# Performance work log

Hardware: AMD Instinct MI355X
Metric: run time of the kernel (lower is better)

The kernel has to match this reference:

```python
import jax, jax.numpy as jnp
import numpy as np

N_FULL = 50000
N_POOL = 12500
E_FULL = 600000
E_POOL = 150000
D = 128


def gcn_conv(x, W, b, edge_index, n):
    """GCNConv with self-loops and symmetric normalization.
    x: [n, d_in], W: [d_in, d_out], edge_index: [2, E] (src -> dst)."""
    xw = x @ W  # [n, d_out]
    loops = jnp.arange(n, dtype=edge_index.dtype)
    src = jnp.concatenate([edge_index[0], loops])
    dst = jnp.concatenate([edge_index[1], loops])
    deg = jnp.zeros((n,), dtype=xw.dtype).at[dst].add(1.0)  # >= 1 (self loops)
    dinv = jax.lax.rsqrt(deg)
    norm = (dinv[src] * dinv[dst])[:, None]  # [E+n, 1]
    out = jax.ops.segment_sum(xw[src] * norm, dst, num_segments=n)
    return out + b


def setup_inputs() -> dict:
    key = jax.random.key(0)
    ks = jax.random.split(key, 8)
    s = 1.0 / np.sqrt(D)
    return {
        "x": jnp.zeros((N_FULL, D), jnp.float32),
        "edge_index": jax.random.randint(ks[0], (2, E_FULL), 0, N_FULL, dtype=jnp.int64)
            if jax.config.jax_enable_x64 else jax.random.randint(ks[0], (2, E_FULL), 0, N_FULL).astype(jnp.int32),
        "pooled_x": jax.random.normal(ks[1], (N_POOL, D), jnp.float32),
        "pooled_edge_index": jax.random.randint(ks[2], (2, E_POOL), 0, N_POOL).astype(jnp.int32),
        "unpool_info": jnp.arange(N_POOL, dtype=jnp.int32),  # unique TopK-kept indices
        "W0": jax.random.normal(ks[3], (D, D), jnp.float32) * s,
        "b0": jnp.zeros((D,), jnp.float32),
        "W1": jax.random.normal(ks[4], (D, D), jnp.float32) * s,
        "b1": jnp.zeros((D,), jnp.float32),
        "W2": jax.random.normal(ks[5], (D, D), jnp.float32) * s,
        "b2": jnp.zeros((D,), jnp.float32),
    }


def reference(x, edge_index, pooled_x, pooled_edge_index, unpool_info,
              W0, b0, W1, b1, W2, b2):
    n = x.shape[0]
    # conv0 on the pooled graph + activation (ELU)
    h = jax.nn.elu(gcn_conv(pooled_x, W0, b0, pooled_edge_index, pooled_x.shape[0]))
    # TopKPool unpool: zero full graph, scatter pooled features to kept indices
    xf = jnp.zeros_like(x).at[unpool_info].set(h)
    # remaining convs on the full graph (dropout=0 / eval mode -> identity)
    xf = jax.nn.elu(gcn_conv(xf, W1, b1, edge_index, n))
    xf = jax.nn.elu(gcn_conv(xf, W2, b2, edge_index, n))
    return xf
```

## Files before the change

### kernel.cpp

```cpp
#include <hip/hip_runtime.h>
#include <math.h>

#define DD 128

static inline int cdiv(long a, long b){ return (int)((a + b - 1) / b); }

typedef __attribute__((ext_vector_type(4))) float f32x4;
typedef __attribute__((ext_vector_type(8))) short bf16x8;
typedef __attribute__((ext_vector_type(4))) short sh4;

__device__ __forceinline__ unsigned short bf16_rn(float f){
  unsigned u = __float_as_uint(f);
  u += 0x7fffu + ((u >> 16) & 1u);
  return (unsigned short)(u >> 16);
}

__global__ void k_count2(const int* __restrict__ dst_f, int Ef, int* __restrict__ cnt_f,
                         int* __restrict__ rank_f,
                         const int* __restrict__ dst_p, int Ep, int* __restrict__ cnt_p,
                         int* __restrict__ rank_p,
                         int* __restrict__ invm, int nf){
  int e = blockIdx.x * blockDim.x + threadIdx.x;
  if (e < Ef){ rank_f[e] = atomicAdd(&cnt_f[dst_f[e]], 1); return; }
  e -= Ef;
  if (e < Ep){ rank_p[e] = atomicAdd(&cnt_p[dst_p[e]], 1); return; }
  e -= Ep;
  if (e < nf) invm[e] = -1;
}

__global__ __launch_bounds__(256) void k_bsum(
    const int* __restrict__ cnt_f, int nf, const int* __restrict__ cnt_p, int np,
    int* __restrict__ bsum_f, int* __restrict__ bsum_p, int nbf, int nbp,
    const int* __restrict__ unpool, int* __restrict__ inv, int npool){
  int bi = blockIdx.x;
  if (bi >= nbf + nbp){
    int i = (bi - nbf - nbp) * 256 + threadIdx.x;
    if (i < npool) inv[unpool[i]] = i;
    return;
  }
  const int* cnt; int n; int* bsum; int b;
  if (bi < nbf){ cnt = cnt_f; n = nf; bsum = bsum_f; b = bi; }
  else         { cnt = cnt_p; n = np; bsum = bsum_p; b = bi - nbf; }
  __shared__ int s[256];
  int t = threadIdx.x;
  long base = (long)b * 1024 + t * 4;
  int v = 0;
  if (base + 3 < n){ int4 q = *(const int4*)(cnt + base); v = q.x + q.y + q.z + q.w; }
  else { for (int j = 0; j < 4; j++) if (base + j < n) v += cnt[base + j]; }
  s[t] = v; __syncthreads();
  for (int off = 128; off > 0; off >>= 1){ if (t < off) s[t] += s[t + off]; __syncthreads(); }
  if (t == 0) bsum[b] = s[0];
}

__global__ __launch_bounds__(128) void k_scan_b(int* __restrict__ bsum_f, int nbf,
                                                int* __restrict__ bsum_p, int nbp){
  __shared__ int s[128];
  int t = threadIdx.x;
  int v = (t < nbf) ? bsum_f[t] : 0;
  s[t] = v; __syncthreads();
  for (int off = 1; off < 128; off <<= 1){ int u = (t >= off) ? s[t - off] : 0; __syncthreads(); s[t] += u; __syncthreads(); }
  if (t < nbf) bsum_f[t] = s[t] - v;
  __syncthreads();
  int v2 = (t < nbp) ? bsum_p[t] : 0;
  s[t] = v2; __syncthreads();
  for (int off = 1; off < 128; off <<= 1){ int u = (t >= off) ? s[t - off] : 0; __syncthreads(); s[t] += u; __syncthreads(); }
  if (t < nbp) bsum_p[t] = s[t] - v2;
}

__global__ __launch_bounds__(256) void k_scan_f(
    const int* __restrict__ cnt_f, int nf, const int* __restrict__ bsum_f,
    const int* __restrict__ cnt_p, int np, const int* __restrict__ bsum_p,
    int* __restrict__ rptr_f, float* __restrict__ dinv_f,
    int* __restrict__ rptr_p, float* __restrict__ dinv_p,
    int nbf, int Ef, int Ep){
  const int* cnt; const int* bsum; int* rptr; float* dinv; int n; int b;
  if ((int)blockIdx.x < nbf){ cnt=cnt_f; bsum=bsum_f; rptr=rptr_f; dinv=dinv_f; n=nf; b=blockIdx.x; }
  else                      { cnt=cnt_p; bsum=bsum_p; rptr=rptr_p; dinv=dinv_p; n=np; b=blockIdx.x-nbf; }
  __shared__ int s[256];
  int t = threadIdx.x;
  long base = (long)b * 1024 + t * 4;
  int c0=0,c1=0,c2=0,c3=0;
  if (base + 3 < n){ int4 q = *(const int4*)(cnt + base); c0=q.x; c1=q.y; c2=q.z; c3=q.w; }
  else {
    if (base + 0 < n) c0 = cnt[base + 0];
    if (base + 1 < n) c1 = cnt[base + 1];
    if (base + 2 < n) c2 = cnt[base + 2];
  }
  int tsum = c0 + c1 + c2 + c3;
  s[t] = tsum; __syncthreads();
  for (int off = 1; off < 256; off <<= 1){ int u = (t >= off) ? s[t - off] : 0; __syncthreads(); s[t] += u; __syncthreads(); }
  int run = bsum[b] + s[t] - tsum;
  int r0 = run, r1 = r0 + c0, r2 = r1 + c1, r3 = r2 + c2;
  if (base + 3 < n){
    *(int4*)(rptr + base) = make_int4(r0, r1, r2, r3);
    dinv[base + 0] = rsqrtf((float)(c0 + 1));
    dinv[base + 1] = rsqrtf((float)(c1 + 1));
    dinv[base + 2] = rsqrtf((float)(c2 + 1));
    dinv[base + 3] = rsqrtf((float)(c3 + 1));
  } else {
    if (base + 0 < n){ rptr[base+0]=r0; dinv[base+0]=rsqrtf((float)(c0+1)); }
    if (base + 1 < n){ rptr[base+1]=r1; dinv[base+1]=rsqrtf((float)(c1+1)); }
    if (base + 2 < n){ rptr[base+2]=r2; dinv[base+2]=rsqrtf((float)(c2+1)); }
  }
  if (blockIdx.x == 0 && t == 0){ rptr_f[nf] = Ef; rptr_p[np] = Ep; }
}

__global__ void k_fill2(const int* __restrict__ src_f, const int* __restrict__ dst_f, int Ef,
                        const int* __restrict__ rptr_f, const int* __restrict__ rank_f,
                        int2* __restrict__ ewk1_f, int2* __restrict__ ewk2_f,
                        const float* __restrict__ dinv_f, const int* __restrict__ inv,
                        const int* __restrict__ src_p, const int* __restrict__ dst_p, int Ep,
                        const int* __restrict__ rptr_p, const int* __restrict__ rank_p,
                        int2* __restrict__ ewk_p,
                        const float* __restrict__ dinv_p){
  int e = blockIdx.x * blockDim.x + threadIdx.x;
  if (e < Ef){
    int s = src_f[e];
    int p = rptr_f[dst_f[e]] + rank_f[e];
    int w = __float_as_int(dinv_f[s]);
    ewk2_f[p] = make_int2(s, w);
    ewk1_f[p] = make_int2(inv[s], w);
  } else {
    e -= Ef;
    if (e < Ep){
      int s = src_p[e];
      int p = rptr_p[dst_p[e]] + rank_p[e];
      ewk_p[p] = make_int2(s, __float_as_int(dinv_p[s]));
    }
  }
}

template <bool BF16OUT>
__global__ __launch_bounds__(256, 2) void k_gemm_mfma(const float* __restrict__ A,
                                                      const float* __restrict__ W,
                                                      void* __restrict__ Cout, int n){
  __shared__ unsigned short Wl[2][16384];
  const int t    = threadIdx.x;
  const int lane = t & 63;
  const int wv   = t >> 6;
  const int g    = lane >> 4;
  const int r    = lane & 15;

  #pragma unroll
  for (int i = 0; i < 4; i++){
    int item = t + i * 256;
    int kq = item >> 5;
    int c4 = item & 31;
    const float* Wp = W + (long)kq * 512 + c4 * 4;
    float4 ww[4];
    #pragma unroll
    for (int kk = 0; kk < 4; kk++) ww[kk] = *(const float4*)(Wp + kk * 128);
    #pragma unroll
    for (int m = 0; m < 4; m++){
      int c = c4 * 4 + m;
      int boff = c * 256 + (((kq >> 1) ^ (c & 15)) * 16) + (kq & 1) * 8;
      sh4 hq, lq;
      #pragma unroll
      for (int kk = 0; kk < 4; kk++){
        float f = ((const float*)&ww[kk])[m];
        unsigned short hh = bf16_rn(f);
        float hf = __uint_as_float((unsigned)hh << 16);
        hq[kk] = (short)hh;
        lq[kk] = (short)bf16_rn(f - hf);
      }
      *(sh4*)((char*)(&Wl[0][0]) + boff) = hq;
      *(sh4*)((char*)(&Wl[1][0]) + boff) = lq;
    }
  }
  __syncthreads();

  const int rb = blockIdx.x * 128 + wv * 32;
  const int r0 = rb + r, r1 = rb + 16 + r;
  const bool v0 = r0 < n, v1 = r1 < n;
  const float* pa0 = A + (long)r0 * DD + g * 8;
  const float* pa1 = A + (long)r1 * DD + g * 8;

  f32x4 acc[2][8];
  #pragma unroll
  for (int i = 0; i < 2; i++)
    #pragma unroll
    for (int j = 0; j < 8; j++){ f32x4 z = {0.f,0.f,0.f,0.f}; acc[i][j] = z; }

  #pragma unroll
  for (int ks = 0; ks < 4; ks++){
    const float4 z4 = make_float4(0.f,0.f,0.f,0.f);
    float4 a00 = v0 ? *(const float4*)(pa0 + ks * 32)     : z4;
    float4 a01 = v0 ? *(const float4*)(pa0 + ks * 32 + 4) : z4;
    float4 a10 = v1 ? *(const float4*)(pa1 + ks * 32)     : z4;
    float4 a11 = v1 ? *(const float4*)(pa1 + ks * 32 + 4) : z4;
    bf16x8 ah0, al0, ah1, al1;
    {
      float f[8] = {a00.x,a00.y,a00.z,a00.w,a01.x,a01.y,a01.z,a01.w};
      #pragma unroll
      for (int i = 0; i < 8; i++){
        unsigned short hh = bf16_rn(f[i]);
        ah0[i] = (short)hh;
        al0[i] = (short)bf16_rn(f[i] - __uint_as_float((unsigned)hh << 16));
      }
    }
    {
      float f[8] = {a10.x,a10.y,a10.z,a10.w,a11.x,a11.y,a11.z,a11.w};
      #pragma unroll
      for (int i = 0; i < 8; i++){
        unsigned short hh = bf16_rn(f[i]);
        ah1[i] = (short)hh;
        al1[i] = (short)bf16_rn(f[i] - __uint_as_float((unsigned)hh << 16));
      }
    }
    const int sb = ks * 4 + g;
    #pragma unroll
    for (int cf = 0; cf < 8; cf++){
      const int boff = (cf * 16 + r) * 256 + ((sb ^ r) * 16);
      bf16x8 wh = *(const bf16x8*)((const char*)(&Wl[0][0]) + boff);
      bf16x8 wl = *(const bf16x8*)((const char*)(&Wl[1][0]) + boff);
      acc[0][cf] = __builtin_amdgcn_mfma_f32_16x16x32_bf16(ah0, wh, acc[0][cf], 0, 0, 0);
      acc[1][cf] = __builtin_amdgcn_mfma_f32_16x16x32_bf16(ah1, wh, acc[1][cf], 0, 0, 0);
      acc[0][cf] = __builtin_amdgcn_mfma_f32_16x16x32_bf16(al0, wh, acc[0][cf], 0, 0, 0);
      acc[1][cf] = __builtin_amdgcn_mfma_f32_16x16x32_bf16(al1, wh, acc[1][cf], 0, 0, 0);
      acc[0][cf] = __builtin_amdgcn_mfma_f32_16x16x32_bf16(ah0, wl, acc[0][cf], 0, 0, 0);
      acc[1][cf] = __builtin_amdgcn_mfma_f32_16x16x32_bf16(ah1, wl, acc[1][cf], 0, 0, 0);
    }
  }

  #pragma unroll
  for (int rf = 0; rf < 2; rf++){
    #pragma unroll
    for (int cf = 0; cf < 8; cf++){
      #pragma unroll
      for (int e = 0; e < 4; e++){
        int row = rb + rf * 16 + g * 4 + e;
        if (row < n){
          float v = acc[rf][cf][e];
          if (BF16OUT)
            ((unsigned short*)Cout)[(long)row * DD + cf * 16 + r] = bf16_rn(v);
          else
            ((float*)Cout)[(long)row * DD + cf * 16 + r] = v;
        }
      }
    }
  }
}

__global__ __launch_bounds__(256) void k_agg_csr(const float* __restrict__ xw,
    const int* __restrict__ rptr, const int2* __restrict__ ewk,
    const float* __restrict__ dinv, const float* __restrict__ b,
    float* __restrict__ out, int n){
  int row = blockIdx.x * 4 + (threadIdx.x >> 6);
  if (row >= n) return;
  int c = (threadIdx.x & 63) * 2;
  int j0 = __builtin_amdgcn_readfirstlane(rptr[row]);
  int j1 = __builtin_amdgcn_readfirstlane(rptr[row + 1]);
  float ax[4], ay[4];
  #pragma unroll
  for (int i = 0; i < 4; i++){ ax[i] = 0.f; ay[i] = 0.f; }
  int j = j0;
  for (; j + 3 < j1; j += 4){
    #pragma unroll
    for (int i = 0; i < 4; i++){
      int2 q = ewk[j + i];
      float w = __int_as_float(q.y);
      float2 v = *(const float2*)(xw + (long)q.x * DD + c);
      ax[i] += v.x * w; ay[i] += v.y * w;
    }
  }
  for (; j < j1; j++){
    int2 q = ewk[j];
    float w = __int_as_float(q.y);
    float2 v = *(const float2*)(xw + (long)q.x * DD + c);
    ax[0] += v.x * w; ay[0] += v.y * w;
  }
  float sax = (ax[0]+ax[1]) + (ax[2]+ax[3]);
  float say = (ay[0]+ay[1]) + (ay[2]+ay[3]);
  float dd = dinv[row];
  float2 sv = *(const float2*)(xw + (long)row * DD + c);
  float2 bb = *(const float2*)(b + c);
  float vx = sax * dd + sv.x * dd * dd + bb.x;
  float vy = say * dd + sv.y * dd * dd + bb.y;
  vx = vx > 0.f ? vx : expm1f(vx);
  vy = vy > 0.f ? vy : expm1f(vy);
  *(float2*)(out + (long)row * DD + c) = make_float2(vx, vy);
}

__global__ __launch_bounds__(256) void k_agg_csr_b(const unsigned short* __restrict__ xwb,
    const int* __restrict__ rptr, const int2* __restrict__ ewk,
    const float* __restrict__ dinv, const float* __restrict__ b,
    float* __restrict__ out, int n){
  int row = blockIdx.x * 4 + (threadIdx.x >> 6);
  if (row >= n) return;
  int c = (threadIdx.x & 63) * 2;
  int j0 = __builtin_amdgcn_readfirstlane(rptr[row]);
  int j1 = __builtin_amdgcn_readfirstlane(rptr[row + 1]);
  float ax[8], ay[8];
  #pragma unroll
  for (int i = 0; i < 8; i++){ ax[i] = 0.f; ay[i] = 0.f; }
  int j = j0;
  for (; j + 7 < j1; j += 8){
    #pragma unroll
    for (int i = 0; i < 8; i++){
      int2 q = ewk[j + i];
      float w = __int_as_float(q.y);
      unsigned v = *(const unsigned*)(xwb + (long)q.x * DD + c);
      ax[i] += __uint_as_float(v << 16) * w;
      ay[i] += __uint_as_float(v & 0xffff0000u) * w;
    }
  }
  for (; j < j1; j++){
    int2 q = ewk[j];
    float w = __int_as_float(q.y);
    unsigned v = *(const unsigned*)(xwb + (long)q.x * DD + c);
    ax[0] += __uint_as_float(v << 16) * w;
    ay[0] += __uint_as_float(v & 0xffff0000u) * w;
  }
  float sax = ((ax[0]+ax[1])+(ax[2]+ax[3])) + ((ax[4]+ax[5])+(ax[6]+ax[7]));
  float say = ((ay[0]+ay[1])+(ay[2]+ay[3])) + ((ay[4]+ay[5])+(ay[6]+ay[7]));
  float dd = dinv[row];
  unsigned sv = *(const unsigned*)(xwb + (long)row * DD + c);
  float sx = __uint_as_float(sv << 16), sy = __uint_as_float(sv & 0xffff0000u);
  float2 bb = *(const float2*)(b + c);
  float vx = sax * dd + sx * dd * dd + bb.x;
  float vy = say * dd + sy * dd * dd + bb.y;
  vx = vx > 0.f ? vx : expm1f(vx);
  vy = vy > 0.f ? vy : expm1f(vy);
  *(float2*)(out + (long)row * DD + c) = make_float2(vx, vy);
}

__global__ __launch_bounds__(256) void k_agg_csr_sp_b(const unsigned short* __restrict__ hwb,
    const int* __restrict__ inv, const int* __restrict__ rptr,
    const int2* __restrict__ ewk,
    const float* __restrict__ dinv, const float* __restrict__ b,
    float* __restrict__ out, int n){
  int row = blockIdx.x * 4 + (threadIdx.x >> 6);
  if (row >= n) return;
  int c = (threadIdx.x & 63) * 2;
  int j0 = __builtin_amdgcn_readfirstlane(rptr[row]);
  int j1 = __builtin_amdgcn_readfirstlane(rptr[row + 1]);
  float ax[8], ay[8];
  #pragma unroll
  for (int i = 0; i < 8; i++){ ax[i] = 0.f; ay[i] = 0.f; }
  int j = j0;
  for (; j + 7 < j1; j += 8){
    #pragma unroll
    for (int i = 0; i < 8; i++){
      int2 q = ewk[j + i];
      float w = __int_as_float(q.y);
      if (q.x >= 0){
        unsigned v = *(const unsigned*)(hwb + (long)q.x * DD + c);
        ax[i] += __uint_as_float(v << 16) * w;
        ay[i] += __uint_as_float(v & 0xffff0000u) * w;
      }
    }
  }
  for (; j < j1; j++){
    int2 q = ewk[j];
    float w = __int_as_float(q.y);
    if (q.x >= 0){
      unsigned v = *(const unsigned*)(hwb + (long)q.x * DD + c);
      ax[0] += __uint_as_float(v << 16) * w;
      ay[0] += __uint_as_float(v & 0xffff0000u) * w;
    }
  }
  float sax = ((ax[0]+ax[1])+(ax[2]+ax[3])) + ((ax[4]+ax[5])+(ax[6]+ax[7]));
  float say = ((ay[0]+ay[1])+(ay[2]+ay[3])) + ((ay[4]+ay[5])+(ay[6]+ay[7]));
  float dd = dinv[row];
  int pr = inv[row];
  float sx = 0.f, sy = 0.f;
  if (pr >= 0){
    unsigned sv = *(const unsigned*)(hwb + (long)pr * DD + c);
    sx = __uint_as_float(sv << 16); sy = __uint_as_float(sv & 0xffff0000u);
  }
  float2 bb = *(const float2*)(b + c);
  float vx = sax * dd + sx * dd * dd + bb.x;
  float vy = say * dd + sy * dd * dd + bb.y;
  vx = vx > 0.f ? vx : expm1f(vx);
  vy = vy > 0.f ? vy : expm1f(vy);
  *(float2*)(out + (long)row * DD + c) = make_float2(vx, vy);
}

extern "C" void kernel_launch(void* const* d_in, const int* in_sizes, int n_in,
                              void* d_out, int out_size, void* d_ws, size_t ws_size,
                              hipStream_t stream) {
  const int*   edge   = (const int*)d_in[1];
  const float* px     = (const float*)d_in[2];
  const int*   pedge  = (const int*)d_in[3];
  const int*   unpool = (const int*)d_in[4];
  const float* W0 = (const float*)d_in[5]; const float* b0 = (const float*)d_in[6];
  const float* W1 = (const float*)d_in[7]; const float* b1 = (const float*)d_in[8];
  const float* W2 = (const float*)d_in[9]; const float* b2 = (const float*)d_in[10];
  const int n_full = in_sizes[0] / DD;
  const int E_full = in_sizes[1] / 2;
  const int n_pool = in_sizes[2] / DD;
  const int E_pool = in_sizes[3] / 2;
  float* out = (float*)d_out;

  char* w = (char*)d_ws;
  size_t off = 0;
  auto alloc = [&](size_t bytes) -> void* {
    void* p = (void*)(w + off);
    off += (bytes + 255) / 256 * 256;
    return p;
  };
  float* dinv_p = (float*)alloc((size_t)n_pool * 4);
  float* dinv_f = (float*)alloc((size_t)n_full * 4);
  int* cnt_p  = (int*)alloc((size_t)n_pool * 4);
  int* cnt_f  = (int*)alloc((size_t)n_full * 4);
  size_t cnt_span = (size_t)((char*)(cnt_f + n_full) - (char*)cnt_p);
  int* rptr_p = (int*)alloc((size_t)(n_pool + 1) * 4);
  int* rptr_f = (int*)alloc((size_t)(n_full + 1) * 4);
  int* rank_p = (int*)alloc((size_t)E_pool * 4);
  int* rank_f = (int*)alloc((size_t)E_full * 4);
  int2* ewk_p  = (int2*)alloc((size_t)E_pool * 8);
  int2* ewk1_f = (int2*)alloc((size_t)E_full * 8);
  int2* ewk2_f = (int2*)alloc((size_t)E_full * 8);
  int* invm   = (int*)alloc((size_t)n_full * 4);
  const int nbf = cdiv(n_full, 1024), nbp = cdiv(n_pool, 1024);
  int* bsum_f = (int*)alloc((size_t)nbf * 4);
  int* bsum_p = (int*)alloc((size_t)nbp * 4);
  const size_t big = (size_t)n_full * DD * 4;
  float* bufA = (float*)alloc(big);
  float* bufB = (float*)alloc(big);

  const int* src_f = edge;          const int* dst_f = edge + E_full;
  const int* src_p = pedge;         const int* dst_p = pedge + E_pool;

  (void)hipMemsetAsync(cnt_p, 0, cnt_span, stream);
  k_count2<<<cdiv((long)E_full + E_pool + n_full,256),256,0,stream>>>(
      dst_f, E_full, cnt_f, rank_f, dst_p, E_pool, cnt_p, rank_p, invm, n_full);
  const int nbi = cdiv(n_pool, 256);
  k_bsum<<<nbf + nbp + nbi,256,0,stream>>>(cnt_f, n_full, cnt_p, n_pool, bsum_f, bsum_p,
                                           nbf, nbp, unpool, invm, n_pool);
  k_scan_b<<<1,128,0,stream>>>(bsum_f, nbf, bsum_p, nbp);
  k_scan_f<<<nbf + nbp,256,0,stream>>>(cnt_f, n_full, bsum_f, cnt_p, n_pool, bsum_p,
                                       rptr_f, dinv_f, rptr_p, dinv_p,
                                       nbf, E_full, E_pool);
  k_fill2<<<cdiv((long)E_full + E_pool,256),256,0,stream>>>(
      src_f, dst_f, E_full, rptr_f, rank_f, ewk1_f, ewk2_f, dinv_f, invm,
      src_p, dst_p, E_pool, rptr_p, rank_p, ewk_p, dinv_p);

  float* xw0 = bufA;
  float* h0  = bufB;
  unsigned short* hw1b = (unsigned short*)bufA;
  float* y1  = bufB;
  unsigned short* xw2b = (unsigned short*)bufA;

  k_gemm_mfma<false><<<cdiv(n_pool,128),256,0,stream>>>(px, W0, xw0, n_pool);
  k_agg_csr<<<cdiv(n_pool,4),256,0,stream>>>(xw0, rptr_p, ewk_p, dinv_p, b0, h0, n_pool);

  k_gemm_mfma<true><<<cdiv(n_pool,128),256,0,stream>>>(h0, W1, hw1b, n_pool);
  k_agg_csr_sp_b<<<cdiv(n_full,4),256,0,stream>>>(hw1b, invm, rptr_f, ewk1_f, dinv_f, b1, y1, n_full);

  k_gemm_mfma<true><<<cdiv(n_full,128),256,0,stream>>>(y1, W2, xw2b, n_full);
  k_agg_csr_b<<<cdiv(n_full,4),256,0,stream>>>(xw2b, rptr_f, ewk2_f, dinv_f, b2, out, n_full);
}
```

Before: 285.1 us.

## Replace CSR build with fixed-capacity padded adjacency and overflow list

Drops the count/scan/fill CSR pipeline in favour of a single scatter kernel that writes each edge source into a fixed 48-slot row per destination, with a small global overflow list for rows past capacity. Degree normalisation is now computed on the fly from counts inside the aggregation kernels instead of stored per edge. Aggregations also emit activations as pre-split bf16 hi/lo pairs, so the following GEMM skips the fp32-to-bf16 split. This removes several small launches and a scan, at the cost of a larger padded buffer, an extra gather of counts per edge, and a linear overflow scan per row that gets expensive if many edges overflow.

```diff
diff --git a/kernel.cpp b/kernel.cpp
--- a/kernel.cpp
+++ b/kernel.cpp
@@ -2,6 +2,9 @@
 #include <math.h>
 
 #define DD 128
+#define CF 48
+#define CP 48
+#define OVF_CAP 4096
 
 static inline int cdiv(long a, long b){ return (int)((a + b - 1) / b); }
 
@@ -15,123 +18,35 @@
   return (unsigned short)(u >> 16);
 }
 
-__global__ void k_count2(const int* __restrict__ dst_f, int Ef, int* __restrict__ cnt_f,
-                         int* __restrict__ rank_f,
-                         const int* __restrict__ dst_p, int Ep, int* __restrict__ cnt_p,
-                         int* __restrict__ rank_p,
-                         int* __restrict__ invm, int nf){
-  int e = blockIdx.x * blockDim.x + threadIdx.x;
-  if (e < Ef){ rank_f[e] = atomicAdd(&cnt_f[dst_f[e]], 1); return; }
-  e -= Ef;
-  if (e < Ep){ rank_p[e] = atomicAdd(&cnt_p[dst_p[e]], 1); return; }
-  e -= Ep;
-  if (e < nf) invm[e] = -1;
-}
-
-__global__ __launch_bounds__(256) void k_bsum(
-    const int* __restrict__ cnt_f, int nf, const int* __restrict__ cnt_p, int np,
-    int* __restrict__ bsum_f, int* __restrict__ bsum_p, int nbf, int nbp,
-    const int* __restrict__ unpool, int* __restrict__ inv, int npool){
-  int bi = blockIdx.x;
-  if (bi >= nbf + nbp){
-    int i = (bi - nbf - nbp) * 256 + threadIdx.x;
-    if (i < npool) inv[unpool[i]] = i;
-    return;
-  }
-  const int* cnt; int n; int* bsum; int b;
-  if (bi < nbf){ cnt = cnt_f; n = nf; bsum = bsum_f; b = bi; }
-  else         { cnt = cnt_p; n = np; bsum = bsum_p; b = bi - nbf; }
-  __shared__ int s[256];
-  int t = threadIdx.x;
-  long base = (long)b * 1024 + t * 4;
-  int v = 0;
-  if (base + 3 < n){ int4 q = *(const int4*)(cnt + base); v = q.x + q.y + q.z + q.w; }
-  else { for (int j = 0; j < 4; j++) if (base + j < n) v += cnt[base + j]; }
-  s[t] = v; __syncthreads();
-  for (int off = 128; off > 0; off >>= 1){ if (t < off) s[t] += s[t + off]; __syncthreads(); }
-  if (t == 0) bsum[b] = s[0];
-}
-
-__global__ __launch_bounds__(128) void k_scan_b(int* __restrict__ bsum_f, int nbf,
-                                                int* __restrict__ bsum_p, int nbp){
-  __shared__ int s[128];
-  int t = threadIdx.x;
-  int v = (t < nbf) ? bsum_f[t] : 0;
-  s[t] = v; __syncthreads();
-  for (int off = 1; off < 128; off <<= 1){ int u = (t >= off) ? s[t - off] : 0; __syncthreads(); s[t] += u; __syncthreads(); }
-  if (t < nbf) bsum_f[t] = s[t] - v;
-  __syncthreads();
-  int v2 = (t < nbp) ? bsum_p[t] : 0;
-  s[t] = v2; __syncthreads();
-  for (int off = 1; off < 128; off <<= 1){ int u = (t >= off) ? s[t - off] : 0; __syncthreads(); s[t] += u; __syncthreads(); }
-  if (t < nbp) bsum_p[t] = s[t] - v2;
-}
-
-__global__ __launch_bounds__(256) void k_scan_f(
-    const int* __restrict__ cnt_f, int nf, const int* __restrict__ bsum_f,
-    const int* __restrict__ cnt_p, int np, const int* __restrict__ bsum_p,
-    int* __restrict__ rptr_f, float* __restrict__ dinv_f,
-    int* __restrict__ rptr_p, float* __restrict__ dinv_p,
-    int nbf, int Ef, int Ep){
-  const int* cnt; const int* bsum; int* rptr; float* dinv; int n; int b;
-  if ((int)blockIdx.x < nbf){ cnt=cnt_f; bsum=bsum_f; rptr=rptr_f; dinv=dinv_f; n=nf; b=blockIdx.x; }
-  else                      { cnt=cnt_p; bsum=bsum_p; rptr=rptr_p; dinv=dinv_p; n=np; b=blockIdx.x-nbf; }
-  __shared__ int s[256];
-  int t = threadIdx.x;
-  long base = (long)b * 1024 + t * 4;
-  int c0=0,c1=0,c2=0,c3=0;
-  if (base + 3 < n){ int4 q = *(const int4*)(cnt + base); c0=q.x; c1=q.y; c2=q.z; c3=q.w; }
-  else {
-    if (base + 0 < n) c0 = cnt[base + 0];
-    if (base + 1 < n) c1 = cnt[base + 1];
-    if (base + 2 < n) c2 = cnt[base + 2];
-  }
-  int tsum = c0 + c1 + c2 + c3;
-  s[t] = tsum; __syncthreads();
-  for (int off = 1; off < 256; off <<= 1){ int u = (t >= off) ? s[t - off] : 0; __syncthreads(); s[t] += u; __syncthreads(); }
-  int run = bsum[b] + s[t] - tsum;
-  int r0 = run, r1 = r0 + c0, r2 = r1 + c1, r3 = r2 + c2;
-  if (base + 3 < n){
-    *(int4*)(rptr + base) = make_int4(r0, r1, r2, r3);
-    dinv[base + 0] = rsqrtf((float)(c0 + 1));
-    dinv[base + 1] = rsqrtf((float)(c1 + 1));
-    dinv[base + 2] = rsqrtf((float)(c2 + 1));
-    dinv[base + 3] = rsqrtf((float)(c3 + 1));
-  } else {
-    if (base + 0 < n){ rptr[base+0]=r0; dinv[base+0]=rsqrtf((float)(c0+1)); }
-    if (base + 1 < n){ rptr[base+1]=r1; dinv[base+1]=rsqrtf((float)(c1+1)); }
-    if (base + 2 < n){ rptr[base+2]=r2; dinv[base+2]=rsqrtf((float)(c2+1)); }
-  }
-  if (blockIdx.x == 0 && t == 0){ rptr_f[nf] = Ef; rptr_p[np] = Ep; }
-}
-
-__global__ void k_fill2(const int* __restrict__ src_f, const int* __restrict__ dst_f, int Ef,
-                        const int* __restrict__ rptr_f, const int* __restrict__ rank_f,
-                        int2* __restrict__ ewk1_f, int2* __restrict__ ewk2_f,
-                        const float* __restrict__ dinv_f, const int* __restrict__ inv,
-                        const int* __restrict__ src_p, const int* __restrict__ dst_p, int Ep,
-                        const int* __restrict__ rptr_p, const int* __restrict__ rank_p,
-                        int2* __restrict__ ewk_p,
-                        const float* __restrict__ dinv_p){
+__global__ void k_scatter(const int* __restrict__ src_f, const int* __restrict__ dst_f, int Ef,
+                          int* __restrict__ cnt_f, int* __restrict__ ewk_f,
+                          int2* __restrict__ ovf_f, int* __restrict__ novf_f,
+                          const int* __restrict__ src_p, const int* __restrict__ dst_p, int Ep,
+                          int* __restrict__ cnt_p, int* __restrict__ ewk_p,
+                          int2* __restrict__ ovf_p, int* __restrict__ novf_p,
+                          const int* __restrict__ unpool, int* __restrict__ inv, int npool){
   int e = blockIdx.x * blockDim.x + threadIdx.x;
   if (e < Ef){
-    int s = src_f[e];
-    int p = rptr_f[dst_f[e]] + rank_f[e];
-    int w = __float_as_int(dinv_f[s]);
-    ewk2_f[p] = make_int2(s, w);
-    ewk1_f[p] = make_int2(inv[s], w);
-  } else {
-    e -= Ef;
-    if (e < Ep){
-      int s = src_p[e];
-      int p = rptr_p[dst_p[e]] + rank_p[e];
-      ewk_p[p] = make_int2(s, __float_as_int(dinv_p[s]));
-    }
-  }
-}
-
-template <bool BF16OUT>
-__global__ __launch_bounds__(256, 2) void k_gemm_mfma(const float* __restrict__ A,
+    int s = src_f[e], d = dst_f[e];
+    int r = atomicAdd(&cnt_f[d], 1);
+    if (r < CF) ewk_f[(long)d * CF + r] = s;
+    else { int o = atomicAdd(novf_f, 1); if (o < OVF_CAP) ovf_f[o] = make_int2(s, d); }
+    return;
+  }
+  e -= Ef;
+  if (e < Ep){
+    int s = src_p[e], d = dst_p[e];
+    int r = atomicAdd(&cnt_p[d], 1);
+    if (r < CP) ewk_p[(long)d * CP + r] = s;
+    else { int o = atomicAdd(novf_p, 1); if (o < OVF_CAP) ovf_p[o] = make_int2(s, d); }
+    return;
+  }
+  e -= Ep;
+  if (e < npool) inv[unpool[e]] = e;
+}
+
+template <int AMODE, bool BF16OUT>
+__global__ __launch_bounds__(256, 2) void k_gemm_mfma(const void* __restrict__ Ap,
                                                       const float* __restrict__ W,
                                                       void* __restrict__ Cout, int n){
   __shared__ unsigned short Wl[2][16384];
@@ -172,8 +87,6 @@
   const int rb = blockIdx.x * 128 + wv * 32;
   const int r0 = rb + r, r1 = rb + 16 + r;
   const bool v0 = r0 < n, v1 = r1 < n;
-  const float* pa0 = A + (long)r0 * DD + g * 8;
-  const float* pa1 = A + (long)r1 * DD + g * 8;
 
   f32x4 acc[2][8];
   #pragma unroll
@@ -183,28 +96,40 @@
 
   #pragma unroll
   for (int ks = 0; ks < 4; ks++){
-    const float4 z4 = make_float4(0.f,0.f,0.f,0.f);
-    float4 a00 = v0 ? *(const float4*)(pa0 + ks * 32)     : z4;
-    float4 a01 = v0 ? *(const float4*)(pa0 + ks * 32 + 4) : z4;
-    float4 a10 = v1 ? *(const float4*)(pa1 + ks * 32)     : z4;
-    float4 a11 = v1 ? *(const float4*)(pa1 + ks * 32 + 4) : z4;
     bf16x8 ah0, al0, ah1, al1;
-    {
-      float f[8] = {a00.x,a00.y,a00.z,a00.w,a01.x,a01.y,a01.z,a01.w};
+    if (AMODE == 0){
+      const float* pa0 = (const float*)Ap + (long)r0 * DD + g * 8;
+      const float* pa1 = (const float*)Ap + (long)r1 * DD + g * 8;
+      const float4 z4 = make_float4(0.f,0.f,0.f,0.f);
+      float4 a00 = v0 ? *(const float4*)(pa0 + ks * 32)     : z4;
+      float4 a01 = v0 ? *(const float4*)(pa0 + ks * 32 + 4) : z4;
+      float4 a10 = v1 ? *(const float4*)(pa1 + ks * 32)     : z4;
+      float4 a11 = v1 ? *(const float4*)(pa1 + ks * 32 + 4) : z4;
+      float f0[8] = {a00.x,a00.y,a00.z,a00.w,a01.x,a01.y,a01.z,a01.w};
+      float f1[8] = {a10.x,a10.y,a10.z,a10.w,a11.x,a11.y,a11.z,a11.w};
       #pragma unroll
       for (int i = 0; i < 8; i++){
-        unsigned short hh = bf16_rn(f[i]);
+        unsigned short hh = bf16_rn(f0[i]);
         ah0[i] = (short)hh;
-        al0[i] = (short)bf16_rn(f[i] - __uint_as_float((unsigned)hh << 16));
-      }
-    }
-    {
-      float f[8] = {a10.x,a10.y,a10.z,a10.w,a11.x,a11.y,a11.z,a11.w};
+        al0[i] = (short)bf16_rn(f0[i] - __uint_as_float((unsigned)hh << 16));
+        unsigned short h1 = bf16_rn(f1[i]);
+        ah1[i] = (short)h1;
+        al1[i] = (short)bf16_rn(f1[i] - __uint_as_float((unsigned)h1 << 16));
+      }
+    } else {
+      const unsigned* qa0 = (const unsigned*)Ap + (long)r0 * DD + g * 8;
+      const unsigned* qa1 = (const unsigned*)Ap + (long)r1 * DD + g * 8;
+      const uint4 z4 = make_uint4(0,0,0,0);
+      uint4 u00 = v0 ? *(const uint4*)(qa0 + ks * 32)     : z4;
+      uint4 u01 = v0 ? *(const uint4*)(qa0 + ks * 32 + 4) : z4;
+      uint4 u10 = v1 ? *(const uint4*)(qa1 + ks * 32)     : z4;
+      uint4 u11 = v1 ? *(const uint4*)(qa1 + ks * 32 + 4) : z4;
+      unsigned uu0[8] = {u00.x,u00.y,u00.z,u00.w,u01.x,u01.y,u01.z,u01.w};
+      unsigned uu1[8] = {u10.x,u10.y,u10.z,u10.w,u11.x,u11.y,u11.z,u11.w};
       #pragma unroll
       for (int i = 0; i < 8; i++){
-        unsigned short hh = bf16_rn(f[i]);
-        ah1[i] = (short)hh;
-        al1[i] = (short)bf16_rn(f[i] - __uint_as_float((unsigned)hh << 16));
+        ah0[i] = (short)(uu0[i] & 0xffffu); al0[i] = (short)(uu0[i] >> 16);
+        ah1[i] = (short)(uu1[i] & 0xffffu); al1[i] = (short)(uu1[i] >> 16);
       }
     }
     const int sb = ks * 4 + g;
@@ -241,133 +166,196 @@
   }
 }
 
-__global__ __launch_bounds__(256) void k_agg_csr(const float* __restrict__ xw,
-    const int* __restrict__ rptr, const int2* __restrict__ ewk,
-    const float* __restrict__ dinv, const float* __restrict__ b,
-    float* __restrict__ out, int n){
+__global__ __launch_bounds__(256) void k_agg0(const float* __restrict__ xw,
+    const int* __restrict__ cnt, const int* __restrict__ ewk,
+    const int2* __restrict__ ovf, const int* __restrict__ novf,
+    const float* __restrict__ b, unsigned* __restrict__ outp, int n){
   int row = blockIdx.x * 4 + (threadIdx.x >> 6);
   if (row >= n) return;
   int c = (threadIdx.x & 63) * 2;
-  int j0 = __builtin_amdgcn_readfirstlane(rptr[row]);
-  int j1 = __builtin_amdgcn_readfirstlane(rptr[row + 1]);
+  int deg = __builtin_amdgcn_readfirstlane(cnt[row]);
+  int m = deg < CP ? deg : CP;
+  long base = (long)row * CP;
   float ax[4], ay[4];
   #pragma unroll
   for (int i = 0; i < 4; i++){ ax[i] = 0.f; ay[i] = 0.f; }
-  int j = j0;
-  for (; j + 3 < j1; j += 4){
+  int j = 0;
+  for (; j + 3 < m; j += 4){
+    int4 ss = *(const int4*)(ewk + base + j);
+    int sa[4] = {ss.x, ss.y, ss.z, ss.w};
     #pragma unroll
     for (int i = 0; i < 4; i++){
-      int2 q = ewk[j + i];
-      float w = __int_as_float(q.y);
-      float2 v = *(const float2*)(xw + (long)q.x * DD + c);
+      int s = sa[i];
+      float w = rsqrtf((float)cnt[s] + 1.f);
+      float2 v = *(const float2*)(xw + (long)s * DD + c);
       ax[i] += v.x * w; ay[i] += v.y * w;
     }
   }
-  for (; j < j1; j++){
-    int2 q = ewk[j];
-    float w = __int_as_float(q.y);
-    float2 v = *(const float2*)(xw + (long)q.x * DD + c);
+  for (; j < m; j++){
+    int s = ewk[base + j];
+    float w = rsqrtf((float)cnt[s] + 1.f);
+    float2 v = *(const float2*)(xw + (long)s * DD + c);
     ax[0] += v.x * w; ay[0] += v.y * w;
+  }
+  int no = __builtin_amdgcn_readfirstlane(novf[0]);
+  if (no > 0){
+    no = no < OVF_CAP ? no : OVF_CAP;
+    for (int k = 0; k < no; k++){
+      int2 od = ovf[k];
+      if (od.y == row){
+        float w = rsqrtf((float)cnt[od.x] + 1.f);
+        float2 v = *(const float2*)(xw + (long)od.x * DD + c);
+        ax[0] += v.x * w; ay[0] += v.y * w;
+      }
+    }
   }
   float sax = (ax[0]+ax[1]) + (ax[2]+ax[3]);
   float say = (ay[0]+ay[1]) + (ay[2]+ay[3]);
-  float dd = dinv[row];
+  float dd = rsqrtf((float)deg + 1.f);
   float2 sv = *(const float2*)(xw + (long)row * DD + c);
   float2 bb = *(const float2*)(b + c);
   float vx = sax * dd + sv.x * dd * dd + bb.x;
   float vy = say * dd + sv.y * dd * dd + bb.y;
   vx = vx > 0.f ? vx : expm1f(vx);
   vy = vy > 0.f ? vy : expm1f(vy);
-  *(float2*)(out + (long)row * DD + c) = make_float2(vx, vy);
-}
-
-__global__ __launch_bounds__(256) void k_agg_csr_b(const unsigned short* __restrict__ xwb,
-    const int* __restrict__ rptr, const int2* __restrict__ ewk,
-    const float* __restrict__ dinv, const float* __restrict__ b,
-    float* __restrict__ out, int n){
+  unsigned short hx = bf16_rn(vx);
+  unsigned short lx = bf16_rn(vx - __uint_as_float((unsigned)hx << 16));
+  unsigned short hy = bf16_rn(vy);
+  unsigned short ly = bf16_rn(vy - __uint_as_float((unsigned)hy << 16));
+  *(uint2*)(outp + (long)row * DD + c) =
+      make_uint2((unsigned)hx | ((unsigned)lx << 16), (unsigned)hy | ((unsigned)ly << 16));
+}
+
+__global__ __launch_bounds__(256) void k_agg1(const unsigned short* __restrict__ hwb,
+    const int* __restrict__ inv, const int* __restrict__ cnt,
+    const int* __restrict__ ewk, const int2* __restrict__ ovf, const int* __restrict__ novf,
+    const float* __restrict__ b, unsigned* __restrict__ outp, int n){
   int row = blockIdx.x * 4 + (threadIdx.x >> 6);
   if (row >= n) return;
   int c = (threadIdx.x & 63) * 2;
-  int j0 = __builtin_amdgcn_readfirstlane(rptr[row]);
-  int j1 = __builtin_amdgcn_readfirstlane(rptr[row + 1]);
+  int deg = __builtin_amdgcn_readfirstlane(cnt[row]);
+  int m = deg < CF ? deg : CF;
+  long base = (long)row * CF;
   float ax[8], ay[8];
   #pragma unroll
   for (int i = 0; i < 8; i++){ ax[i] = 0.f; ay[i] = 0.f; }
-  int j = j0;
-  for (; j + 7 < j1; j += 8){
+  int j = 0;
+  for (; j + 7 < m; j += 8){
+    int4 s0 = *(const int4*)(ewk + base + j);
+    int4 s1 = *(const int4*)(ewk + base + j + 4);
+    int sa[8] = {s0.x, s0.y, s0.z, s0.w, s1.x, s1.y, s1.z, s1.w};
     #pragma unroll
     for (int i = 0; i < 8; i++){
-      int2 q = ewk[j + i];
-      float w = __int_as_float(q.y);
-      unsigned v = *(const unsigned*)(xwb + (long)q.x * DD + c);
-      ax[i] += __uint_as_float(v << 16) * w;
-      ay[i] += __uint_as_float(v & 0xffff0000u) * w;
-    }
-  }
-  for (; j < j1; j++){
-    int2 q = ewk[j];
-    float w = __int_as_float(q.y);
-    unsigned v = *(const unsigned*)(xwb + (long)q.x * DD + c);
-    ax[0] += __uint_as_float(v << 16) * w;
-    ay[0] += __uint_as_float(v & 0xffff0000u) * w;
+      int s = sa[i];
+      int pr = inv[s];
+      if (pr >= 0){
+        float w = rsqrtf((float)cnt[s] + 1.f);
+        unsigned v = *(const unsigned*)(hwb + (long)pr * DD + c);
+        ax[i] += __uint_as_float(v << 16) * w;
+        ay[i] += __uint_as_float(v & 0xffff0000u) * w;
+      }
+    }
+  }
+  for (; j < m; j++){
+    int s = ewk[base + j];
+    int pr = inv[s];
+    if (pr >= 0){
+      float w = rsqrtf((float)cnt[s] + 1.f);
+      unsigned v = *(const unsigned*)(hwb + (long)pr * DD + c);
+      ax[0] += __uint_as_float(v << 16) * w;
+      ay[0] += __uint_as_float(v & 0xffff0000u) * w;
+    }
+  }
+  int no = __builtin_amdgcn_readfirstlane(novf[0]);
+  if (no > 0){
+    no = no < OVF_CAP ? no : OVF_CAP;
+    for (int k = 0; k < no; k++){
+      int2 od = ovf[k];
+      if (od.y == row){
+        int pr = inv[od.x];
+        if (pr >= 0){
+          float w = rsqrtf((float)cnt[od.x] + 1.f);
+          unsigned v = *(const unsigned*)(hwb + (long)pr * DD + c);
+          ax[0] += __uint_as_float(v << 16) * w;
+          ay[0] += __uint_as_float(v & 0xffff0000u) * w;
+        }
+      }
+    }
   }
   float sax = ((ax[0]+ax[1])+(ax[2]+ax[3])) + ((ax[4]+ax[5])+(ax[6]+ax[7]));
   float say = ((ay[0]+ay[1])+(ay[2]+ay[3])) + ((ay[4]+ay[5])+(ay[6]+ay[7]));
-  float dd = dinv[row];
-  unsigned sv = *(const unsigned*)(xwb + (long)row * DD + c);
-  float sx = __uint_as_float(sv << 16), sy = __uint_as_float(sv & 0xffff0000u);
+  float dd = rsqrtf((float)deg + 1.f);
+  int pr = inv[row];
+  float sx = 0.f, sy = 0.f;
+  if (pr >= 0){
+    unsigned sv = *(const unsigned*)(hwb + (long)pr * DD + c);
+    sx = __uint_as_float(sv << 16); sy = __uint_as_float(sv & 0xffff0000u);
+  }
   float2 bb = *(const float2*)(b + c);
   float vx = sax * dd + sx * dd * dd + bb.x;
   float vy = say * dd + sy * dd * dd + bb.y;
   vx = vx > 0.f ? vx : expm1f(vx);
   vy = vy > 0.f ? vy : expm1f(vy);
-  *(float2*)(out + (long)row * DD + c) = make_float2(vx, vy);
-}
-
-__global__ __launch_bounds__(256) void k_agg_csr_sp_b(const unsigned short* __restrict__ hwb,
-    const int* __restrict__ inv, const int* __restrict__ rptr,
-    const int2* __restrict__ ewk,
-    const float* __restrict__ dinv, const float* __restrict__ b,
-    float* __restrict__ out, int n){
+  unsigned short hx = bf16_rn(vx);
+  unsigned short lx = bf16_rn(vx - __uint_as_float((unsigned)hx << 16));
+  unsigned short hy = bf16_rn(vy);
+  unsigned short ly = bf16_rn(vy - __uint_as_float((unsigned)hy << 16));
+  *(uint2*)(outp + (long)row * DD + c) =
+      make_uint2((unsigned)hx | ((unsigned)lx << 16), (unsigned)hy | ((unsigned)ly << 16));
+}
+
+__global__ __launch_bounds__(256) void k_agg2(const unsigned short* __restrict__ xwb,
+    const int* __restrict__ cnt, const int* __restrict__ ewk,
+    const int2* __restrict__ ovf, const int* __restrict__ novf,
+    const float* __restrict__ b, float* __restrict__ out, int n){
   int row = blockIdx.x * 4 + (threadIdx.x >> 6);
   if (row >= n) return;
   int c = (threadIdx.x & 63) * 2;
-  int j0 = __builtin_amdgcn_readfirstlane(rptr[row]);
-  int j1 = __builtin_amdgcn_readfirstlane(rptr[row + 1]);
+  int deg = __builtin_amdgcn_readfirstlane(cnt[row]);
+  int m = deg < CF ? deg : CF;
+  long base = (long)row * CF;
   float ax[8], ay[8];
   #pragma unroll
   for (int i = 0; i < 8; i++){ ax[i] = 0.f; ay[i] = 0.f; }
-  int j = j0;
-  for (; j + 7 < j1; j += 8){
+  int j = 0;
+  for (; j + 7 < m; j += 8){
+    int4 s0 = *(const int4*)(ewk + base + j);
+    int4 s1 = *(const int4*)(ewk + base + j + 4);
+    int sa[8] = {s0.x, s0.y, s0.z, s0.w, s1.x, s1.y, s1.z, s1.w};
     #pragma unroll
     for (int i = 0; i < 8; i++){
-      int2 q = ewk[j + i];
-      float w = __int_as_float(q.y);
-      if (q.x >= 0){
-        unsigned v = *(const unsigned*)(hwb + (long)q.x * DD + c);
-        ax[i] += __uint_as_float(v << 16) * w;
-        ay[i] += __uint_as_float(v & 0xffff0000u) * w;
-      }
-    }
-  }
-  for (; j < j1; j++){
-    int2 q = ewk[j];
-    float w = __int_as_float(q.y);
-    if (q.x >= 0){
-      unsigned v = *(const unsigned*)(hwb + (long)q.x * DD + c);
-      ax[0] += __uint_as_float(v << 16) * w;
-      ay[0] += __uint_as_float(v & 0xffff0000u) * w;
+      int s = sa[i];
+      float w = rsqrtf((float)cnt[s] + 1.f);
+      unsigned v = *(const unsigned*)(xwb + (long)s * DD + c);
+      ax[i] += __uint_as_float(v << 16) * w;
+      ay[i] += __uint_as_float(v & 0xffff0000u) * w;
+    }
+  }
+  for (; j < m; j++){
+    int s = ewk[base + j];
+    float w = rsqrtf((float)cnt[s] + 1.f);
+    unsigned v = *(const unsigned*)(xwb + (long)s * DD + c);
+    ax[0] += __uint_as_float(v << 16) * w;
+    ay[0] += __uint_as_float(v & 0xffff0000u) * w;
+  }
+  int no = __builtin_amdgcn_readfirstlane(novf[0]);
+  if (no > 0){
+    no = no < OVF_CAP ? no : OVF_CAP;
+    for (int k = 0; k < no; k++){
+      int2 od = ovf[k];
+      if (od.y == row){
+        float w = rsqrtf((float)cnt[od.x] + 1.f);
+        unsigned v = *(const unsigned*)(xwb + (long)od.x * DD + c);
+        ax[0] += __uint_as_float(v << 16) * w;
+        ay[0] += __uint_as_float(v & 0xffff0000u) * w;
+      }
     }
   }
   float sax = ((ax[0]+ax[1])+(ax[2]+ax[3])) + ((ax[4]+ax[5])+(ax[6]+ax[7]));
   float say = ((ay[0]+ay[1])+(ay[2]+ay[3])) + ((ay[4]+ay[5])+(ay[6]+ay[7]));
-  float dd = dinv[row];
-  int pr = inv[row];
-  float sx = 0.f, sy = 0.f;
-  if (pr >= 0){
-    unsigned sv = *(const unsigned*)(hwb + (long)pr * DD + c);
-    sx = __uint_as_float(sv << 16); sy = __uint_as_float(sv & 0xffff0000u);
-  }
+  float dd = rsqrtf((float)deg + 1.f);
+  unsigned sv = *(const unsigned*)(xwb + (long)row * DD + c);
+  float sx = __uint_as_float(sv << 16), sy = __uint_as_float(sv & 0xffff0000u);
   float2 bb = *(const float2*)(b + c);
   float vx = sax * dd + sx * dd * dd + bb.x;
   float vy = say * dd + sy * dd * dd + bb.y;
@@ -399,22 +387,15 @@
     off += (bytes + 255) / 256 * 256;
     return p;
   };
-  float* dinv_p = (float*)alloc((size_t)n_pool * 4);
-  float* dinv_f = (float*)alloc((size_t)n_full * 4);
   int* cnt_p  = (int*)alloc((size_t)n_pool * 4);
   int* cnt_f  = (int*)alloc((size_t)n_full * 4);
-  size_t cnt_span = (size_t)((char*)(cnt_f + n_full) - (char*)cnt_p);
-  int* rptr_p = (int*)alloc((size_t)(n_pool + 1) * 4);
-  int* rptr_f = (int*)alloc((size_t)(n_full + 1) * 4);
-  int* rank_p = (int*)alloc((size_t)E_pool * 4);
-  int* rank_f = (int*)alloc((size_t)E_full * 4);
-  int2* ewk_p  = (int2*)alloc((size_t)E_pool * 8);
-  int2* ewk1_f = (int2*)alloc((size_t)E_full * 8);
-  int2* ewk2_f = (int2*)alloc((size_t)E_full * 8);
+  int* novf2  = (int*)alloc(8);
+  size_t zspan = (size_t)((char*)(novf2 + 2) - (char*)cnt_p);
   int* invm   = (int*)alloc((size_t)n_full * 4);
-  const int nbf = cdiv(n_full, 1024), nbp = cdiv(n_pool, 1024);
-  int* bsum_f = (int*)alloc((size_t)nbf * 4);
-  int* bsum_p = (int*)alloc((size_t)nbp * 4);
+  int* ewk_p  = (int*)alloc((size_t)n_pool * CP * 4);
+  int* ewk_f  = (int*)alloc((size_t)n_full * CF * 4);
+  int2* ovf_p = (int2*)alloc((size_t)OVF_CAP * 8);
+  int2* ovf_f = (int2*)alloc((size_t)OVF_CAP * 8);
   const size_t big = (size_t)n_full * DD * 4;
   float* bufA = (float*)alloc(big);
   float* bufB = (float*)alloc(big);
@@ -422,32 +403,25 @@
   const int* src_f = edge;          const int* dst_f = edge + E_full;
   const int* src_p = pedge;         const int* dst_p = pedge + E_pool;
 
-  (void)hipMemsetAsync(cnt_p, 0, cnt_span, stream);
-  k_count2<<<cdiv((long)E_full + E_pool + n_full,256),256,0,stream>>>(
-      dst_f, E_full, cnt_f, rank_f, dst_p, E_pool, cnt_p, rank_p, invm, n_full);
-  const int nbi = cdiv(n_pool, 256);
-  k_bsum<<<nbf + nbp + nbi,256,0,stream>>>(cnt_f, n_full, cnt_p, n_pool, bsum_f, bsum_p,
-                                           nbf, nbp, unpool, invm, n_pool);
-  k_scan_b<<<1,128,0,stream>>>(bsum_f, nbf, bsum_p, nbp);
-  k_scan_f<<<nbf + nbp,256,0,stream>>>(cnt_f, n_full, bsum_f, cnt_p, n_pool, bsum_p,
-                                       rptr_f, dinv_f, rptr_p, dinv_p,
-                                       nbf, E_full, E_pool);
-  k_fill2<<<cdiv((long)E_full + E_pool,256),256,0,stream>>>(
-      src_f, dst_f, E_full, rptr_f, rank_f, ewk1_f, ewk2_f, dinv_f, invm,
-      src_p, dst_p, E_pool, rptr_p, rank_p, ewk_p, dinv_p);
-
-  float* xw0 = bufA;
-  float* h0  = bufB;
-  unsigned short* hw1b = (unsigned short*)bufA;
-  float* y1  = bufB;
-  unsigned short* xw2b = (unsigned short*)bufA;
-
-  k_gemm_mfma<false><<<cdiv(n_pool,128),256,0,stream>>>(px, W0, xw0, n_pool);
-  k_agg_csr<<<cdiv(n_pool,4),256,0,stream>>>(xw0, rptr_p, ewk_p, dinv_p, b0, h0, n_pool);
-
-  k_gemm_mfma<true><<<cdiv(n_pool,128),256,0,stream>>>(h0, W1, hw1b, n_pool);
-  k_agg_csr_sp_b<<<cdiv(n_full,4),256,0,stream>>>(hw1b, invm, rptr_f, ewk1_f, dinv_f, b1, y1, n_full);
-
-  k_gemm_mfma<true><<<cdiv(n_full,128),256,0,stream>>>(y1, W2, xw2b, n_full);
-  k_agg_csr_b<<<cdiv(n_full,4),256,0,stream>>>(xw2b, rptr_f, ewk2_f, dinv_f, b2, out, n_full);
-}
+  (void)hipMemsetAsync(cnt_p, 0, zspan, stream);
+  (void)hipMemsetAsync(invm, 0xFF, (size_t)n_full * 4, stream);
+  k_scatter<<<cdiv((long)E_full + E_pool + n_pool, 256), 256, 0, stream>>>(
+      src_f, dst_f, E_full, cnt_f, ewk_f, ovf_f, novf2 + 1,
+      src_p, dst_p, E_pool, cnt_p, ewk_p, ovf_p, novf2 + 0,
+      unpool, invm, n_pool);
+
+  float* xw0            = bufA;
+  unsigned* h0p         = (unsigned*)bufB;
+  unsigned short* hw1b  = (unsigned short*)bufA;
+  unsigned* y1p         = (unsigned*)bufB;
+  unsigned short* xw2b  = (unsigned short*)bufA;
+
+  k_gemm_mfma<0,false><<<cdiv(n_pool,128),256,0,stream>>>(px, W0, xw0, n_pool);
+  k_agg0<<<cdiv(n_pool,4),256,0,stream>>>(xw0, cnt_p, ewk_p, ovf_p, novf2 + 0, b0, h0p, n_pool);
+
+  k_gemm_mfma<1,true><<<cdiv(n_pool,128),256,0,stream>>>(h0p, W1, hw1b, n_pool);
+  k_agg1<<<cdiv(n_full,4),256,0,stream>>>(hw1b, invm, cnt_f, ewk_f, ovf_f, novf2 + 1, b1, y1p, n_full);
+
+  k_gemm_mfma<1,true><<<cdiv(n_full,128),256,0,stream>>>(y1p, W2, xw2b, n_full);
+  k_agg2<<<cdiv(n_full,4),256,0,stream>>>(xw2b, cnt_f, ewk_f, ovf_f, novf2 + 1, b2, out, n_full);
+}
```

Measured after the change: 297.4 us. 4.3% more time.
